# Performance work log

Hardware: AMD Instinct MI355X
Metric: run time of the kernel (lower is better)

## Reference

```python
import jax, jax.numpy as jnp
import numpy as np

DIM = 256
HEADS = 8
HEAD_DIM = 32
WS = 64
MLP = 1024
INNER = HEADS * HEAD_DIM
EPS = 1e-5


def setup_inputs() -> dict:
    key = jax.random.key(0)
    ks = jax.random.split(key, 10)
    B, N = 2, 65536
    s = lambda fan_in: 1.0 / np.sqrt(fan_in)
    return {
        "x": jax.random.normal(ks[0], (B, N, DIM), jnp.float32),
        "w_qkv": jax.random.normal(ks[1], (DIM, 3 * INNER), jnp.float32) * s(DIM),
        "w_out": jax.random.normal(ks[2], (INNER, DIM), jnp.float32) * s(INNER),
        "b_out": jnp.zeros((DIM,), jnp.float32),
        "pos_emb": jax.random.normal(ks[3], (WS, WS), jnp.float32),
        "ln1_g": jnp.ones((DIM,), jnp.float32),
        "ln1_b": jnp.zeros((DIM,), jnp.float32),
        "w1": jax.random.normal(ks[4], (DIM, MLP), jnp.float32) * s(DIM),
        "b1": jnp.zeros((MLP,), jnp.float32),
        "w2": jax.random.normal(ks[5], (MLP, DIM), jnp.float32) * s(MLP),
        "b2": jnp.zeros((DIM,), jnp.float32),
        "ln2_g": jnp.ones((DIM,), jnp.float32),
        "ln2_b": jnp.zeros((DIM,), jnp.float32),
    }


def layernorm(x, g, b):
    mu = jnp.mean(x, axis=-1, keepdims=True)
    var = jnp.var(x, axis=-1, keepdims=True)
    return (x - mu) * jax.lax.rsqrt(var + EPS) * g + b


def window_attn(x, w_qkv, w_out, b_out, pos_emb):
    # shifted window attention (displacement = WS // 2)
    disp = WS // 2
    x = jnp.roll(x, -disp, axis=1)
    b, n, _ = x.shape
    n_w = n // WS
    qkv = x @ w_qkv  # [b, n, 3*inner]
    qkv = qkv.reshape(b, n_w, WS, 3, HEADS, HEAD_DIM)
    q = jnp.transpose(qkv[:, :, :, 0], (0, 3, 1, 2, 4))  # [b, h, n_w, ws, d]
    k = jnp.transpose(qkv[:, :, :, 1], (0, 3, 1, 2, 4))
    v = jnp.transpose(qkv[:, :, :, 2], (0, 3, 1, 2, 4))
    scale = HEAD_DIM ** -0.5
    dots = jnp.einsum("bhwid,bhwjd->bhwij", q, k) * scale + pos_emb
    attn = jax.nn.softmax(dots, axis=-1)
    out = jnp.einsum("bhwij,bhwjd->bhwid", attn, v)
    out = jnp.transpose(out, (0, 2, 3, 1, 4)).reshape(b, n, INNER)
    out = out @ w_out + b_out
    return jnp.roll(out, disp, axis=1)


def reference(x, w_qkv, w_out, b_out, pos_emb, ln1_g, ln1_b, w1, b1, w2, b2, ln2_g, ln2_b):
    # PointSwinBlock: Residual(PreNorm(attn)) then Residual(PreNorm(ffn))
    x = x + window_attn(layernorm(x, ln1_g, ln1_b), w_qkv, w_out, b_out, pos_emb)
    h = layernorm(x, ln2_g, ln2_b)
    h = jax.nn.gelu(h @ w1 + b1, approximate=False) @ w2 + b2
    return x + h
```

## Files before the change

### kernel.cpp

```cpp
#include <hip/hip_runtime.h>
#include <hip/hip_bf16.h>
#include <math.h>
#include <stdint.h>

#define DIM   256
#define NSEQ  65536
#define NTOK  131072
#define HEADS 8
#define HD    32
#define WSZ   64
#define NWIN  2048
#define QKVN  768
#define MLPD  1024
#define LNEPS 1e-5f

typedef __bf16 bf16;
typedef __bf16 bf16x8 __attribute__((ext_vector_type(8)));
typedef __bf16 bf16x4 __attribute__((ext_vector_type(4)));
typedef float  f32x4  __attribute__((ext_vector_type(4)));

__device__ __forceinline__ int roll_row(int r) {
  return (r & 0x10000) | ((r + 32) & 0xFFFF);
}

__device__ __forceinline__ float fast_gelu(float v) {
  const float x2 = v * v;
  const float z2 = v * __builtin_fmaf(x2, 0.07135481630268f, 1.5957691216057308f);
  const float e  = __expf(z2);
  const float r  = __builtin_amdgcn_rcpf(e + 1.0f);
  return __builtin_fmaf(-v, r, v);
}

template<int NY>
__device__ __forceinline__ void grid_swz(int& mBase, int& nBase) {
  const int nwg  = gridDim.x;
  const int lin  = blockIdx.x;
  const int orig = (lin & 7) * (nwg >> 3) + (lin >> 3);
  mBase = (orig / NY) * 128;
  nBase = (orig % NY) * 128;
}

__device__ __forceinline__ void stage16(const bf16* g, bf16* l) {
#if __has_builtin(__builtin_amdgcn_global_load_lds)
  __builtin_amdgcn_global_load_lds((const __attribute__((address_space(1))) void*)g,
                                   (__attribute__((address_space(3))) void*)l, 16, 0, 0);
#else
  int lane = threadIdx.x & 63;
  *(uint4*)((char*)l + lane * 16) = *(const uint4*)g;
#endif
}

template<int K, int LDB, bool ROLL>
__device__ __forceinline__ void gemm_tile(const bf16* __restrict__ A,
                                          const bf16* __restrict__ Bt,
                                          int mBase, int nBase,
                                          bf16* sA, bf16* sB,
                                          f32x4 acc[4][4])
{
  const int tid  = threadIdx.x;
  const int wave = tid >> 6;
  const int lane = tid & 63;
  const int slot = lane & 3;
  const int swz  = (lane >> 3) & 3;
  const int rloc = lane >> 2;
  const int chunk = ((slot ^ swz) * 8);

  int lr0 = mBase + wave * 32 + rloc;
  int lr1 = lr0 + 16;
  int ar0 = ROLL ? roll_row(lr0) : lr0;
  int ar1 = ROLL ? roll_row(lr1) : lr1;
  const bf16* gA0 = A + (size_t)ar0 * K + chunk;
  const bf16* gA1 = A + (size_t)ar1 * K + chunk;
  const bf16* gB0 = Bt + (size_t)(nBase + wave * 32 + rloc) * LDB + chunk;
  const bf16* gB1 = Bt + (size_t)(nBase + wave * 32 + rloc + 16) * LDB + chunk;

  bf16* dA0 = sA + (wave * 32 +  0) * 32;
  bf16* dA1 = sA + (wave * 32 + 16) * 32;
  bf16* dB0 = sB + (wave * 32 +  0) * 32;
  bf16* dB1 = sB + (wave * 32 + 16) * 32;

  const int m0 = (wave & 1) * 64;
  const int n0 = (wave >> 1) * 64;
  const int c    = lane & 15;
  const int quad = lane >> 4;

  int fa[4], fb[4];
#pragma unroll
  for (int t = 0; t < 4; ++t) {
    int rowA = m0 + t * 16 + c;
    fa[t] = rowA * 32 + ((quad ^ ((rowA >> 1) & 3)) * 8);
    int rowB = n0 + t * 16 + c;
    fb[t] = rowB * 32 + ((quad ^ ((rowB >> 1) & 3)) * 8);
  }

  const f32x4 fzero = {0.f, 0.f, 0.f, 0.f};
#pragma unroll
  for (int i = 0; i < 4; ++i)
#pragma unroll
    for (int j = 0; j < 4; ++j) acc[i][j] = fzero;

  for (int k0 = 0; k0 < K; k0 += 32) {
    stage16(gA0 + k0, dA0);
    stage16(gA1 + k0, dA1);
    stage16(gB0 + k0, dB0);
    stage16(gB1 + k0, dB1);
    __syncthreads();
    bf16x8 afr[4], bfr[4];
#pragma unroll
    for (int t = 0; t < 4; ++t) {
      afr[t] = *(const bf16x8*)(sA + fa[t]);
      bfr[t] = *(const bf16x8*)(sB + fb[t]);
    }
#pragma unroll
    for (int i = 0; i < 4; ++i)
#pragma unroll
      for (int j = 0; j < 4; ++j)
        acc[i][j] = __builtin_amdgcn_mfma_f32_16x16x32_bf16(afr[i], bfr[j], acc[i][j], 0, 0, 0);
    __syncthreads();
  }
}

__global__ __launch_bounds__(256) void k_prep(const float* __restrict__ wqkv,
                                              const float* __restrict__ wout,
                                              const float* __restrict__ w1,
                                              const float* __restrict__ w2,
                                              const float* __restrict__ pos,
                                              bf16* __restrict__ wqkvT, bf16* __restrict__ woutT,
                                              bf16* __restrict__ w1T, bf16* __restrict__ w2T,
                                              float* __restrict__ posP)
{
  const int total = 768 * 256 + 256 * 256 + 1024 * 256 + 256 * 1024 + 4096;
  for (int i = blockIdx.x * 256 + threadIdx.x; i < total; i += gridDim.x * 256) {
    int j = i;
    if (j < 768 * 256) { int n = j >> 8, k = j & 255; wqkvT[j] = (bf16)wqkv[k * 768 + n]; continue; }
    j -= 768 * 256;
    if (j < 256 * 256) { int n = j >> 8, k = j & 255; woutT[j] = (bf16)wout[k * 256 + n]; continue; }
    j -= 256 * 256;
    if (j < 1024 * 256) { int n = j >> 8, k = j & 255; w1T[j] = (bf16)w1[k * 1024 + n]; continue; }
    j -= 1024 * 256;
    if (j < 256 * 1024) { int n = j >> 10, k = j & 1023; w2T[j] = (bf16)w2[k * 256 + n]; continue; }
    j -= 256 * 1024;
    {
      int lane = j & 63, t = j >> 6;
      int nt = t & 3, r = (t >> 2) & 3, mt = t >> 4;
      int ii = mt * 16 + (lane >> 4) * 4 + r, jj = nt * 16 + (lane & 15);
      posP[j] = pos[ii * 64 + jj];
    }
  }
}

__global__ __launch_bounds__(256) void k_ln(const float* __restrict__ x,
                                            const float* __restrict__ gam,
                                            const float* __restrict__ bet,
                                            bf16* __restrict__ out)
{
  const int wave = threadIdx.x >> 6, lane = threadIdx.x & 63;
  const int token = blockIdx.x * 4 + wave;
  const float4 v = ((const float4*)x)[(size_t)token * 64 + lane];
  float s = v.x + v.y + v.z + v.w;
  float q = v.x * v.x + v.y * v.y + v.z * v.z + v.w * v.w;
#pragma unroll
  for (int off = 32; off; off >>= 1) { s += __shfl_xor(s, off); q += __shfl_xor(q, off); }
  const float mu = s * (1.f / 256.f);
  const float var = q * (1.f / 256.f) - mu * mu;
  const float rs = rsqrtf(var + LNEPS);
  const float4 gv = ((const float4*)gam)[lane];
  const float4 bv = ((const float4*)bet)[lane];
  bf16x4 o;
  o[0] = (bf16)((v.x - mu) * rs * gv.x + bv.x);
  o[1] = (bf16)((v.y - mu) * rs * gv.y + bv.y);
  o[2] = (bf16)((v.z - mu) * rs * gv.z + bv.z);
  o[3] = (bf16)((v.w - mu) * rs * gv.w + bv.w);
  *(bf16x4*)(out + (size_t)token * 256 + lane * 4) = o;
}

__global__ __launch_bounds__(256, 2) void k_gemm_qkv(const bf16* __restrict__ h1,
                                                     const bf16* __restrict__ wqkvT,
                                                     bf16* __restrict__ qkv)
{
  __shared__ __align__(16) bf16 sA[128 * 32];
  __shared__ __align__(16) bf16 sB[128 * 32];
  f32x4 acc[4][4];
  int mBase, nBase;
  grid_swz<6>(mBase, nBase);
  gemm_tile<256, 256, true>(h1, wqkvT, mBase, nBase, sA, sB, acc);
  const int lane = threadIdx.x & 63, wave = threadIdx.x >> 6;
  const int c = lane & 15, quad = lane >> 4;
  const int rowBase = mBase + (wave & 1) * 64 + quad * 4;
  const int colBase = nBase + (wave >> 1) * 64 + c;
#pragma unroll
  for (int i = 0; i < 4; ++i)
#pragma unroll
    for (int j = 0; j < 4; ++j)
#pragma unroll
      for (int r = 0; r < 4; ++r)
        qkv[(size_t)(rowBase + i * 16 + r) * QKVN + (colBase + j * 16)] = (bf16)acc[i][j][r];
}

__global__ __launch_bounds__(256, 2) void k_attn(const bf16* __restrict__ qkv,
                                                 const float* __restrict__ posP,
                                                 bf16* __restrict__ attn)
{
  __shared__ __align__(16) bf16 sQ[4][64 * 40];
  __shared__ __align__(16) bf16 sK[4][64 * 40];
  __shared__ __align__(16) bf16 sV[4][32 * 72];
  const int tid = threadIdx.x;
  const int wave = tid >> 6, lane = tid & 63;
  const int gh = blockIdx.y * 4 + wave;
  const int win = blockIdx.x;
  const int c = lane & 15, quad = lane >> 4;
  const size_t base = (size_t)win * 64 * QKVN;

  {
    const int row = lane >> 2;
    const int col = (lane & 3) * 8;
#pragma unroll
    for (int i = 0; i < 4; ++i) {
      int rr = i * 16 + row;
      *(uint4*)(&sQ[wave][rr * 40 + col]) = *(const uint4*)(qkv + base + (size_t)rr * QKVN + gh * 32 + col);
      *(uint4*)(&sK[wave][rr * 40 + col]) = *(const uint4*)(qkv + base + (size_t)rr * QKVN + 256 + gh * 32 + col);
    }
  }
  {
    const int d = lane & 31, jh = lane >> 5;
#pragma unroll
    for (int it = 0; it < 32; ++it) {
      int j = it * 2 + jh;
      sV[wave][d * 72 + j] = qkv[base + (size_t)j * QKVN + 512 + gh * 32 + d];
    }
  }

  const f32x4 fzero = {0.f, 0.f, 0.f, 0.f};
  f32x4 sacc[4][4];
#pragma unroll
  for (int i = 0; i < 4; ++i)
#pragma unroll
    for (int j = 0; j < 4; ++j) sacc[i][j] = fzero;
  bf16x8 qf[4], kf[4];
#pragma unroll
  for (int t = 0; t < 4; ++t) {
    qf[t] = *(const bf16x8*)(&sQ[wave][(t * 16 + c) * 40 + quad * 8]);
    kf[t] = *(const bf16x8*)(&sK[wave][(t * 16 + c) * 40 + quad * 8]);
  }
#pragma unroll
  for (int i = 0; i < 4; ++i)
#pragma unroll
    for (int j = 0; j < 4; ++j)
      sacc[i][j] = __builtin_amdgcn_mfma_f32_16x16x32_bf16(qf[i], kf[j], sacc[i][j], 0, 0, 0);

  const float scale = 0.17677669529663687f;
  float p[4][4][4];
#pragma unroll
  for (int i = 0; i < 4; ++i)
#pragma unroll
    for (int j = 0; j < 4; ++j)
#pragma unroll
      for (int r = 0; r < 4; ++r)
        p[i][j][r] = sacc[i][j][r] * scale + posP[(((i * 4 + r) * 4 + j) << 6) + lane];

  float mx[4][4], rcp[4][4];
#pragma unroll
  for (int i = 0; i < 4; ++i)
#pragma unroll
    for (int r = 0; r < 4; ++r) {
      float m = fmaxf(fmaxf(p[i][0][r], p[i][1][r]), fmaxf(p[i][2][r], p[i][3][r]));
      m = fmaxf(m, __shfl_xor(m, 1)); m = fmaxf(m, __shfl_xor(m, 2));
      m = fmaxf(m, __shfl_xor(m, 4)); m = fmaxf(m, __shfl_xor(m, 8));
      mx[i][r] = m;
    }
#pragma unroll
  for (int i = 0; i < 4; ++i)
#pragma unroll
    for (int r = 0; r < 4; ++r) {
#pragma unroll
      for (int j = 0; j < 4; ++j) p[i][j][r] = __expf(p[i][j][r] - mx[i][r]);
      float t = p[i][0][r] + p[i][1][r] + p[i][2][r] + p[i][3][r];
      t += __shfl_xor(t, 1); t += __shfl_xor(t, 2); t += __shfl_xor(t, 4); t += __shfl_xor(t, 8);
      rcp[i][r] = 1.0f / t;
    }
#pragma unroll
  for (int i = 0; i < 4; ++i)
#pragma unroll
    for (int j = 0; j < 4; ++j)
#pragma unroll
      for (int r = 0; r < 4; ++r) p[i][j][r] *= rcp[i][r];

  f32x4 oacc[4][2];
#pragma unroll
  for (int i = 0; i < 4; ++i) { oacc[i][0] = fzero; oacc[i][1] = fzero; }
#pragma unroll
  for (int half = 0; half < 2; ++half) {
#pragma unroll
    for (int i = 0; i < 4; ++i)
#pragma unroll
      for (int j2 = 0; j2 < 2; ++j2)
#pragma unroll
        for (int r = 0; r < 4; ++r)
          sQ[wave][(i * 16 + quad * 4 + r) * 40 + j2 * 16 + c] = (bf16)p[i][half * 2 + j2][r];
    bf16x8 pf[4], vf[2];
#pragma unroll
    for (int t = 0; t < 4; ++t)
      pf[t] = *(const bf16x8*)(&sQ[wave][(t * 16 + c) * 40 + quad * 8]);
#pragma unroll
    for (int n2 = 0; n2 < 2; ++n2)
      vf[n2] = *(const bf16x8*)(&sV[wave][(n2 * 16 + c) * 72 + half * 32 + quad * 8]);
#pragma unroll
    for (int i = 0; i < 4; ++i)
#pragma unroll
      for (int n2 = 0; n2 < 2; ++n2)
        oacc[i][n2] = __builtin_amdgcn_mfma_f32_16x16x32_bf16(pf[i], vf[n2], oacc[i][n2], 0, 0, 0);
  }

#pragma unroll
  for (int i = 0; i < 4; ++i)
#pragma unroll
    for (int n2 = 0; n2 < 2; ++n2)
#pragma unroll
      for (int r = 0; r < 4; ++r)
        attn[(size_t)(win * 64 + i * 16 + quad * 4 + r) * DIM + gh * 32 + n2 * 16 + c] = (bf16)oacc[i][n2][r];
}

__global__ __launch_bounds__(256, 2) void k_gemm_proj(const bf16* __restrict__ attn,
                                                      const bf16* __restrict__ woutT,
                                                      const float* __restrict__ x,
                                                      const float* __restrict__ b_out,
                                                      float* __restrict__ x2)
{
  __shared__ __align__(16) bf16 sA[128 * 32];
  __shared__ __align__(16) bf16 sB[128 * 32];
  f32x4 acc[4][4];
  int mBase, nBase;
  grid_swz<2>(mBase, nBase);
  gemm_tile<256, 256, false>(attn, woutT, mBase, nBase, sA, sB, acc);
  const int lane = threadIdx.x & 63, wave = threadIdx.x >> 6;
  const int c = lane & 15, quad = lane >> 4;
  const int rowBase = mBase + (wave & 1) * 64 + quad * 4;
  const int colBase = nBase + (wave >> 1) * 64 + c;
#pragma unroll
  for (int i = 0; i < 4; ++i)
#pragma unroll
    for (int r = 0; r < 4; ++r) {
      const int rp = rowBase + i * 16 + r;
      const size_t rowoff = (size_t)roll_row(rp) * DIM;
#pragma unroll
      for (int j = 0; j < 4; ++j) {
        const int col = colBase + j * 16;
        x2[rowoff + col] = acc[i][j][r] + b_out[col] + x[rowoff + col];
      }
    }
}

__global__ __launch_bounds__(256, 2) void k_gemm_mlp1(const bf16* __restrict__ h2,
                                                      const bf16* __restrict__ w1Th,
                                                      const float* __restrict__ b1h,
                                                      bf16* __restrict__ g)
{
  __shared__ __align__(16) bf16 sA[128 * 32];
  __shared__ __align__(16) bf16 sB[128 * 32];
  f32x4 acc[4][4];
  int mBase, nBase;
  grid_swz<4>(mBase, nBase);
  gemm_tile<256, 256, false>(h2, w1Th, mBase, nBase, sA, sB, acc);
  const int lane = threadIdx.x & 63, wave = threadIdx.x >> 6;
  const int c = lane & 15, quad = lane >> 4;
  const int rowBase = mBase + (wave & 1) * 64 + quad * 4;
  const int colBase = nBase + (wave >> 1) * 64 + c;
#pragma unroll
  for (int i = 0; i < 4; ++i)
#pragma unroll
    for (int j = 0; j < 4; ++j) {
      const int col = colBase + j * 16;
      const float bb = b1h[col];
#pragma unroll
      for (int r = 0; r < 4; ++r) {
        const float v = acc[i][j][r] + bb;
        g[(size_t)(rowBase + i * 16 + r) * 512 + col] = (bf16)fast_gelu(v);
      }
    }
}

__global__ __launch_bounds__(256, 2) void k_gemm_mlp2(const bf16* __restrict__ g,
                                                      const bf16* __restrict__ w2Th,
                                                      const float* __restrict__ b2,
                                                      float* __restrict__ out,
                                                      int first)
{
  __shared__ __align__(16) bf16 sA[128 * 32];
  __shared__ __align__(16) bf16 sB[128 * 32];
  f32x4 acc[4][4];
  int mBase, nBase;
  grid_swz<2>(mBase, nBase);
  gemm_tile<512, 1024, false>(g, w2Th, mBase, nBase, sA, sB, acc);
  const int lane = threadIdx.x & 63, wave = threadIdx.x >> 6;
  const int c = lane & 15, quad = lane >> 4;
  const int rowBase = mBase + (wave & 1) * 64 + quad * 4;
  const int colBase = nBase + (wave >> 1) * 64 + c;
#pragma unroll
  for (int i = 0; i < 4; ++i)
#pragma unroll
    for (int j = 0; j < 4; ++j) {
      const int col = colBase + j * 16;
      const float bb = first ? b2[col] : 0.0f;
#pragma unroll
      for (int r = 0; r < 4; ++r) {
        const size_t off = (size_t)(rowBase + i * 16 + r) * DIM + col;
        out[off] = out[off] + acc[i][j][r] + bb;
      }
    }
}

extern "C" void kernel_launch(void* const* d_in, const int* in_sizes, int n_in,
                              void* d_out, int out_size, void* d_ws, size_t ws_size,
                              hipStream_t stream) {
  const float* x    = (const float*)d_in[0];
  const float* wqkv = (const float*)d_in[1];
  const float* wout = (const float*)d_in[2];
  const float* bo   = (const float*)d_in[3];
  const float* pos  = (const float*)d_in[4];
  const float* l1g  = (const float*)d_in[5];
  const float* l1b  = (const float*)d_in[6];
  const float* w1   = (const float*)d_in[7];
  const float* b1   = (const float*)d_in[8];
  const float* w2   = (const float*)d_in[9];
  const float* b2   = (const float*)d_in[10];
  const float* l2g  = (const float*)d_in[11];
  const float* l2b  = (const float*)d_in[12];
  float* out = (float*)d_out;

  char* ws = (char*)d_ws;
  bf16* h1   = (bf16*)ws;
  bf16* qkv  = (bf16*)(ws + 67108864);
  bf16* attn = h1;
  bf16* h2   = qkv;
  bf16* gbuf = (bf16*)(ws + 134217728);
  char* wp = ws + 268435456;
  bf16* wqkvT = (bf16*)wp;  wp += 768 * 256 * 2;
  bf16* woutT = (bf16*)wp;  wp += 256 * 256 * 2;
  bf16* w1T   = (bf16*)wp;  wp += 1024 * 256 * 2;
  bf16* w2T   = (bf16*)wp;  wp += 256 * 1024 * 2;
  float* posP = (float*)wp;

  k_prep<<<dim3(1024), dim3(256), 0, stream>>>(wqkv, wout, w1, w2, pos, wqkvT, woutT, w1T, w2T, posP);
  k_ln<<<dim3(NTOK / 4), dim3(256), 0, stream>>>(x, l1g, l1b, h1);
  k_gemm_qkv<<<dim3(6144), dim3(256), 0, stream>>>(h1, wqkvT, qkv);
  k_attn<<<dim3(NWIN, 2), dim3(256), 0, stream>>>(qkv, posP, attn);
  k_gemm_proj<<<dim3(2048), dim3(256), 0, stream>>>(attn, woutT, x, bo, out);
  k_ln<<<dim3(NTOK / 4), dim3(256), 0, stream>>>(out, l2g, l2b, h2);
  for (int half = 0; half < 2; ++half) {
    k_gemm_mlp1<<<dim3(4096), dim3(256), 0, stream>>>(h2, w1T + half * 512 * 256, b1 + half * 512, gbuf);
    k_gemm_mlp2<<<dim3(2048), dim3(256), 0, stream>>>(gbuf, w2T + half * 512, b2, out, half == 0 ? 1 : 0);
  }
}
```

Before: 863.7 us.

## Double-buffer GEMM LDS tiles and run MLP in one pass when workspace allows

The shared GEMM tile loop now uses two LDS buffers. It prefetches the next K-slice while computing the current one, which removes one barrier per iteration and overlaps global loads with MFMA work. This doubles LDS per block (32 KB), which may reduce occupancy. Separately, when the workspace is large enough, the MLP runs as a single full-width mlp1 plus a K=1024 mlp2 instead of two halves. That avoids a second read-modify-write of the output, at the cost of a larger intermediate buffer.

```diff
diff --git a/kernel.cpp b/kernel.cpp
--- a/kernel.cpp
+++ b/kernel.cpp
@@ -99,17 +99,28 @@
 #pragma unroll
     for (int j = 0; j < 4; ++j) acc[i][j] = fzero;
 
+  stage16(gA0, dA0);
+  stage16(gA1, dA1);
+  stage16(gB0, dB0);
+  stage16(gB1, dB1);
+  __syncthreads();
+
+  int cur = 0;
   for (int k0 = 0; k0 < K; k0 += 32) {
-    stage16(gA0 + k0, dA0);
-    stage16(gA1 + k0, dA1);
-    stage16(gB0 + k0, dB0);
-    stage16(gB1 + k0, dB1);
-    __syncthreads();
+    const int nxt = cur ^ 1;
+    if (k0 + 32 < K) {
+      const int o = nxt * 4096;
+      stage16(gA0 + k0 + 32, dA0 + o);
+      stage16(gA1 + k0 + 32, dA1 + o);
+      stage16(gB0 + k0 + 32, dB0 + o);
+      stage16(gB1 + k0 + 32, dB1 + o);
+    }
+    const int co = cur * 4096;
     bf16x8 afr[4], bfr[4];
 #pragma unroll
     for (int t = 0; t < 4; ++t) {
-      afr[t] = *(const bf16x8*)(sA + fa[t]);
-      bfr[t] = *(const bf16x8*)(sB + fb[t]);
+      afr[t] = *(const bf16x8*)(sA + co + fa[t]);
+      bfr[t] = *(const bf16x8*)(sB + co + fb[t]);
     }
 #pragma unroll
     for (int i = 0; i < 4; ++i)
@@ -117,6 +128,7 @@
       for (int j = 0; j < 4; ++j)
         acc[i][j] = __builtin_amdgcn_mfma_f32_16x16x32_bf16(afr[i], bfr[j], acc[i][j], 0, 0, 0);
     __syncthreads();
+    cur = nxt;
   }
 }
 
@@ -178,8 +190,8 @@
                                                      const bf16* __restrict__ wqkvT,
                                                      bf16* __restrict__ qkv)
 {
-  __shared__ __align__(16) bf16 sA[128 * 32];
-  __shared__ __align__(16) bf16 sB[128 * 32];
+  __shared__ __align__(16) bf16 sA[2 * 128 * 32];
+  __shared__ __align__(16) bf16 sB[2 * 128 * 32];
   f32x4 acc[4][4];
   int mBase, nBase;
   grid_swz<6>(mBase, nBase);
@@ -326,8 +338,8 @@
                                                       const float* __restrict__ b_out,
                                                       float* __restrict__ x2)
 {
-  __shared__ __align__(16) bf16 sA[128 * 32];
-  __shared__ __align__(16) bf16 sB[128 * 32];
+  __shared__ __align__(16) bf16 sA[2 * 128 * 32];
+  __shared__ __align__(16) bf16 sB[2 * 128 * 32];
   f32x4 acc[4][4];
   int mBase, nBase;
   grid_swz<2>(mBase, nBase);
@@ -350,16 +362,17 @@
     }
 }
 
+template<int LDC, int NY>
 __global__ __launch_bounds__(256, 2) void k_gemm_mlp1(const bf16* __restrict__ h2,
                                                       const bf16* __restrict__ w1Th,
                                                       const float* __restrict__ b1h,
                                                       bf16* __restrict__ g)
 {
-  __shared__ __align__(16) bf16 sA[128 * 32];
-  __shared__ __align__(16) bf16 sB[128 * 32];
+  __shared__ __align__(16) bf16 sA[2 * 128 * 32];
+  __shared__ __align__(16) bf16 sB[2 * 128 * 32];
   f32x4 acc[4][4];
   int mBase, nBase;
-  grid_swz<4>(mBase, nBase);
+  grid_swz<NY>(mBase, nBase);
   gemm_tile<256, 256, false>(h2, w1Th, mBase, nBase, sA, sB, acc);
   const int lane = threadIdx.x & 63, wave = threadIdx.x >> 6;
   const int c = lane & 15, quad = lane >> 4;
@@ -374,23 +387,24 @@
 #pragma unroll
       for (int r = 0; r < 4; ++r) {
         const float v = acc[i][j][r] + bb;
-        g[(size_t)(rowBase + i * 16 + r) * 512 + col] = (bf16)fast_gelu(v);
+        g[(size_t)(rowBase + i * 16 + r) * LDC + col] = (bf16)fast_gelu(v);
       }
     }
 }
 
+template<int K>
 __global__ __launch_bounds__(256, 2) void k_gemm_mlp2(const bf16* __restrict__ g,
                                                       const bf16* __restrict__ w2Th,
                                                       const float* __restrict__ b2,
                                                       float* __restrict__ out,
                                                       int first)
 {
-  __shared__ __align__(16) bf16 sA[128 * 32];
-  __shared__ __align__(16) bf16 sB[128 * 32];
+  __shared__ __align__(16) bf16 sA[2 * 128 * 32];
+  __shared__ __align__(16) bf16 sB[2 * 128 * 32];
   f32x4 acc[4][4];
   int mBase, nBase;
   grid_swz<2>(mBase, nBase);
-  gemm_tile<512, 1024, false>(g, w2Th, mBase, nBase, sA, sB, acc);
+  gemm_tile<K, 1024, false>(g, w2Th, mBase, nBase, sA, sB, acc);
   const int lane = threadIdx.x & 63, wave = threadIdx.x >> 6;
   const int c = lane & 15, quad = lane >> 4;
   const int rowBase = mBase + (wave & 1) * 64 + quad * 4;
@@ -428,12 +442,26 @@
   float* out = (float*)d_out;
 
   char* ws = (char*)d_ws;
+  const size_t WEIGHTS_SZ = (size_t)768 * 256 * 2 + 256 * 256 * 2 + 1024 * 256 * 2
+                          + 256 * 1024 * 2 + 4096 * 4;
+  const size_t FUSED_NEED = 67108864ull + 268435456ull + WEIGHTS_SZ;
+  const bool fused = ws_size >= FUSED_NEED;
+
   bf16* h1   = (bf16*)ws;
   bf16* qkv  = (bf16*)(ws + 67108864);
   bf16* attn = h1;
-  bf16* h2   = qkv;
-  bf16* gbuf = (bf16*)(ws + 134217728);
-  char* wp = ws + 268435456;
+  bf16* h2;
+  bf16* gbuf;
+  char* wp;
+  if (fused) {
+    h2   = (bf16*)ws;
+    gbuf = (bf16*)(ws + 67108864);
+    wp   = ws + 67108864 + 268435456;
+  } else {
+    h2   = qkv;
+    gbuf = (bf16*)(ws + 134217728);
+    wp   = ws + 268435456;
+  }
   bf16* wqkvT = (bf16*)wp;  wp += 768 * 256 * 2;
   bf16* woutT = (bf16*)wp;  wp += 256 * 256 * 2;
   bf16* w1T   = (bf16*)wp;  wp += 1024 * 256 * 2;
@@ -446,8 +474,13 @@
   k_attn<<<dim3(NWIN, 2), dim3(256), 0, stream>>>(qkv, posP, attn);
   k_gemm_proj<<<dim3(2048), dim3(256), 0, stream>>>(attn, woutT, x, bo, out);
   k_ln<<<dim3(NTOK / 4), dim3(256), 0, stream>>>(out, l2g, l2b, h2);
-  for (int half = 0; half < 2; ++half) {
-    k_gemm_mlp1<<<dim3(4096), dim3(256), 0, stream>>>(h2, w1T + half * 512 * 256, b1 + half * 512, gbuf);
-    k_gemm_mlp2<<<dim3(2048), dim3(256), 0, stream>>>(gbuf, w2T + half * 512, b2, out, half == 0 ? 1 : 0);
-  }
-}
+  if (fused) {
+    k_gemm_mlp1<1024, 8><<<dim3(8192), dim3(256), 0, stream>>>(h2, w1T, b1, gbuf);
+    k_gemm_mlp2<1024><<<dim3(2048), dim3(256), 0, stream>>>(gbuf, w2T, b2, out, 1);
+  } else {
+    for (int half = 0; half < 2; ++half) {
+      k_gemm_mlp1<512, 4><<<dim3(4096), dim3(256), 0, stream>>>(h2, w1T + half * 512 * 256, b1 + half * 512, gbuf);
+      k_gemm_mlp2<512><<<dim3(2048), dim3(256), 0, stream>>>(gbuf, w2T + half * 512, b2, out, half == 0 ? 1 : 0);
+    }
+  }
+}
```

New measurement: 797.5 us. 1.08x faster.
